# Optimization experiments

Hardware: AMD Instinct MI355X
Metric: run time of the kernel (lower is better)

The kernel has to match this reference:

```python
import jax, jax.numpy as jnp
import numpy as np

NEG_SLOPE = 0.2  # PyG GATConv default negative_slope
BN_EPS = 1e-5


def gat_layer(x, src, dst, W, b, a_src, a_dst, heads, out_ch, concat):
    # x: [N, Fin]; W: [Fin, heads*out_ch]; a_src/a_dst: [heads, out_ch]
    N = x.shape[0]
    h = (x @ W).reshape(N, heads, out_ch)
    s = (h * a_src).sum(-1)            # [N, H]
    d = (h * a_dst).sum(-1)            # [N, H]
    e = jax.nn.leaky_relu(s[src] + d[dst], NEG_SLOPE)   # [E, H]
    # segment softmax over incoming edges of each destination node
    m = jax.ops.segment_max(e, dst, num_segments=N)
    ex = jnp.exp(e - m[dst])
    denom = jax.ops.segment_sum(ex, dst, num_segments=N)
    alpha = ex / (denom[dst] + 1e-16)                   # [E, H]
    out = jax.ops.segment_sum(alpha[:, :, None] * h[src], dst, num_segments=N)  # [N,H,C]
    out = out.reshape(N, heads * out_ch) if concat else out.mean(axis=1)
    return out + b


def batchnorm(x, gamma, beta):
    mu = x.mean(axis=0)
    var = x.var(axis=0)
    return gamma * (x - mu) * jax.lax.rsqrt(var + BN_EPS) + beta


def setup_inputs() -> dict:
    key = jax.random.key(0)
    ks = jax.random.split(key, 24)
    N, E, Fin, Hd, heads, C = 50000, 800000, 128, 64, 4, 2
    wdim = Hd * heads  # 256
    inp = {
        'x': jax.random.normal(ks[0], (N, Fin), jnp.float32),
        'edge_index': jax.random.randint(ks[1], (2, E), 0, N, jnp.int64),
    }
    def glorot(k, shape):
        fan = shape[0] + shape[-1]
        return jax.random.normal(k, shape, jnp.float32) * np.sqrt(2.0 / fan)
    # layer 0: Fin -> heads x Hd (concat)
    inp['W0'] = glorot(ks[2], (Fin, wdim)); inp['b0'] = jnp.zeros((wdim,), jnp.float32)
    inp['asrc0'] = glorot(ks[3], (heads, Hd)); inp['adst0'] = glorot(ks[4], (heads, Hd))
    inp['g0'] = jnp.ones((wdim,), jnp.float32); inp['be0'] = jnp.zeros((wdim,), jnp.float32)
    # layer 1: wdim -> heads x Hd (concat)
    inp['W1'] = glorot(ks[5], (wdim, wdim)); inp['b1'] = jnp.zeros((wdim,), jnp.float32)
    inp['asrc1'] = glorot(ks[6], (heads, Hd)); inp['adst1'] = glorot(ks[7], (heads, Hd))
    inp['g1'] = jnp.ones((wdim,), jnp.float32); inp['be1'] = jnp.zeros((wdim,), jnp.float32)
    # layer 2: wdim -> 1 head x Hd (no concat)
    inp['W2'] = glorot(ks[8], (wdim, Hd)); inp['b2'] = jnp.zeros((Hd,), jnp.float32)
    inp['asrc2'] = glorot(ks[9], (1, Hd)); inp['adst2'] = glorot(ks[10], (1, Hd))
    inp['g2'] = jnp.ones((Hd,), jnp.float32); inp['be2'] = jnp.zeros((Hd,), jnp.float32)
    # classifier: Linear(2*Hd, Hd) -> ReLU -> Linear(Hd, C)
    inp['Wc1'] = glorot(ks[11], (2 * Hd, Hd)); inp['bc1'] = jnp.zeros((Hd,), jnp.float32)
    inp['Wc2'] = glorot(ks[12], (Hd, C)); inp['bc2'] = jnp.zeros((C,), jnp.float32)
    return inp


def reference(x, edge_index, W0, b0, asrc0, adst0, g0, be0,
              W1, b1, asrc1, adst1, g1, be1,
              W2, b2, asrc2, adst2, g2, be2,
              Wc1, bc1, Wc2, bc2):
    N = x.shape[0]
    # add self-loops (PyG GATConv default)
    loops = jnp.arange(N, dtype=edge_index.dtype)
    src = jnp.concatenate([edge_index[0], loops])
    dst = jnp.concatenate([edge_index[1], loops])
    heads, Hd = asrc0.shape[0], asrc0.shape[1]

    h = gat_layer(x, src, dst, W0, b0, asrc0, adst0, heads, Hd, True)
    h = jax.nn.relu(batchnorm(h, g0, be0))
    h = gat_layer(h, src, dst, W1, b1, asrc1, adst1, heads, Hd, True)
    h = jax.nn.relu(batchnorm(h, g1, be1))
    h = gat_layer(h, src, dst, W2, b2, asrc2, adst2, 1, Hd, False)
    h = jax.nn.relu(batchnorm(h, g2, be2))

    pooled = jnp.concatenate([h.mean(axis=0, keepdims=True),
                              h.max(axis=0, keepdims=True)], axis=1)  # [1, 2*Hd]
    z = jax.nn.relu(pooled @ Wc1 + bc1)
    return z @ Wc2 + bc2  # [1, num_classes]
```

## Files before the change

kernel.cpp:

```cpp
#include <hip/hip_runtime.h>


typedef unsigned int uint;
typedef unsigned short ushort;

#define NEG_SLOPE 0.2f
#define BN_EPS 1e-5f
#define NB_RED 256

typedef __attribute__((ext_vector_type(2))) float f32x2;

__device__ __forceinline__ float bf2f(uint u) { return __uint_as_float(u << 16); }
__device__ __forceinline__ ushort f2bf(float f) {
    uint u = __float_as_uint(f);
    u += 0x7fff + ((u >> 16) & 1);
    return (ushort)(u >> 16);
}


__global__ void prep_kernel(const float* __restrict__ x, ushort* __restrict__ xb,
                            int total_real, int total_pad,
                            const float* __restrict__ W0, ushort* __restrict__ w0t,
                            const float* __restrict__ W1, ushort* __restrict__ w1t,
                            const float* __restrict__ W2, ushort* __restrict__ w2t,
                            const int* __restrict__ ei, int* __restrict__ deg, int E) {
    int i = blockIdx.x * blockDim.x + threadIdx.x;
    if (i < total_pad) {
        xb[i] = (i < total_real) ? f2bf(x[i]) : (ushort)0;
        return;
    }
    int j = i - total_pad;
    if (j < 32768) {
        int n = j / 128, k = j - n * 128;
        w0t[j] = f2bf(W0[(size_t)k * 256 + n]);
        return;
    }
    j -= 32768;
    if (j < 65536) {
        int n = j / 256, k = j - n * 256;
        w1t[j] = f2bf(W1[(size_t)k * 256 + n]);
        return;
    }
    j -= 65536;
    if (j < 16384) {
        int n = j / 256, k = j - n * 256;
        w2t[j] = f2bf(W2[(size_t)k * 64 + n]);
        return;
    }
    j -= 16384;
    if (j < E) atomicAdd(&deg[ei[E + j]], 1);
}


__global__ void scan_part(const int* __restrict__ deg, int* __restrict__ offsets,
                          int* __restrict__ bsum, int N) {
    __shared__ int sh[256];
    int t = threadIdx.x;
    int base = blockIdx.x * 1024 + t * 4;
    int v0 = (base + 0 < N) ? deg[base + 0] : 0;
    int v1 = (base + 1 < N) ? deg[base + 1] : 0;
    int v2 = (base + 2 < N) ? deg[base + 2] : 0;
    int v3 = (base + 3 < N) ? deg[base + 3] : 0;
    int s = v0 + v1 + v2 + v3;
    sh[t] = s;
    __syncthreads();
    for (int off = 1; off < 256; off <<= 1) {
        int y = (t >= off) ? sh[t - off] : 0;
        __syncthreads();
        sh[t] += y;
        __syncthreads();
    }
    int p = sh[t] - s;
    if (base + 0 < N) offsets[base + 0] = p;
    p += v0;
    if (base + 1 < N) offsets[base + 1] = p;
    p += v1;
    if (base + 2 < N) offsets[base + 2] = p;
    p += v2;
    if (base + 3 < N) offsets[base + 3] = p;
    if (t == 255) bsum[blockIdx.x] = sh[255];
}

__global__ void scan_top(const int* __restrict__ bsum, int* __restrict__ bexcl,
                         int nb, int* __restrict__ offsets, int N) {
    if (threadIdx.x == 0) {
        int run = 0;
        for (int b = 0; b < nb; ++b) { bexcl[b] = run; run += bsum[b]; }
        offsets[N] = run;
    }
}

__global__ void scan_add(int* __restrict__ offsets, int* __restrict__ cursor,
                         const int* __restrict__ bexcl, int N) {
    int add = bexcl[blockIdx.x];
    int base = blockIdx.x * 1024 + threadIdx.x * 4;
#pragma unroll
    for (int k = 0; k < 4; ++k) {
        int i = base + k;
        if (i < N) { int v = offsets[i] + add; offsets[i] = v; cursor[i] = v; }
    }
}

__global__ void scatter_kernel(const int* __restrict__ ei, int* __restrict__ cursor,
                               int* __restrict__ srcs, int E) {
    int e = blockIdx.x * blockDim.x + threadIdx.x;
    if (e < E) {
        int s = ei[e];
        int d = ei[E + e];
        int p = atomicAdd(&cursor[d], 1);
        srcs[p] = s;
    }
}


typedef __attribute__((ext_vector_type(8))) short bf16x8;
typedef __attribute__((ext_vector_type(4))) float floatx4;

template <int BN, int H>
__launch_bounds__(256)
__global__ void mfma_gemm_bt(const ushort* __restrict__ A, const ushort* __restrict__ Bt,
                             ushort* __restrict__ C, const float* __restrict__ asrc,
                             const float* __restrict__ adst, float* __restrict__ sv,
                             float* __restrict__ dv, int K, int Nn) {
    constexpr int WCOLS = (BN == 128) ? 2 : 1;
    constexpr int WROWS = 4 / WCOLS;
    constexpr int MT = 128 / (WROWS * 16);
    constexpr int NT = BN / (WCOLS * 16);
    constexpr int BCALLS = (BN * 32 * 2) / 4096;

    __shared__ ushort As[128 * 32];
    __shared__ ushort Bs[BN * 32];

    int t = threadIdx.x;
    int w = t >> 6, l = t & 63;

    int rb, cb;
    if (BN == 128) {
        int nbr = (int)gridDim.x >> 1;
        int full = (nbr & ~7) << 1;
        int id = blockIdx.x;
        if (id < full) {
            rb = ((id >> 4) << 3) + (id & 7);
            cb = (id >> 3) & 1;
        } else {
            int o = id - full;
            int rem = nbr & 7;
            rb = (nbr & ~7) + (rem ? (o % rem) : 0);
            cb = rem ? (o / rem) : 0;
        }
    } else {
        rb = blockIdx.x;
        cb = 0;
    }
    int row0 = rb * 128;
    int col0 = cb * BN;
    int wr = (w / WCOLS) * (MT * 16);
    int wc = (w % WCOLS) * (NT * 16);

    floatx4 acc[MT][NT];
#pragma unroll
    for (int mi = 0; mi < MT; ++mi)
#pragma unroll
        for (int ni = 0; ni < NT; ++ni)
#pragma unroll
            for (int r = 0; r < 4; ++r) acc[mi][ni][r] = 0.f;

    int mrow = l & 15;
    int kc = (l >> 4) * 8;

    for (int kt = 0; kt < K; kt += 32) {
#pragma unroll
        for (int c = 0; c < 2; ++c) {
            int idx = c * 256 + t;
            const ushort* gp = A + (size_t)(row0 + (idx >> 2)) * K + kt + (idx & 3) * 8;
            __builtin_amdgcn_global_load_lds(
                (const __attribute__((address_space(1))) void*)gp,
                (__attribute__((address_space(3))) void*)(As + (idx & ~63) * 8),
                16, 0, 0);
        }
#pragma unroll
        for (int c = 0; c < BCALLS; ++c) {
            int idx = c * 256 + t;
            const ushort* gp = Bt + (size_t)(col0 + (idx >> 2)) * K + kt + (idx & 3) * 8;
            __builtin_amdgcn_global_load_lds(
                (const __attribute__((address_space(1))) void*)gp,
                (__attribute__((address_space(3))) void*)(Bs + (idx & ~63) * 8),
                16, 0, 0);
        }
        __syncthreads();

        bf16x8 af[MT], bfr[NT];
#pragma unroll
        for (int mi = 0; mi < MT; ++mi)
            af[mi] = *(const bf16x8*)&As[(wr + mi * 16 + mrow) * 32 + kc];
#pragma unroll
        for (int ni = 0; ni < NT; ++ni)
            bfr[ni] = *(const bf16x8*)&Bs[(wc + ni * 16 + mrow) * 32 + kc];
#pragma unroll
        for (int mi = 0; mi < MT; ++mi)
#pragma unroll
            for (int ni = 0; ni < NT; ++ni)
                acc[mi][ni] = __builtin_amdgcn_mfma_f32_16x16x32_bf16(
                    af[mi], bfr[ni], acc[mi][ni], 0, 0, 0);
        __syncthreads();
    }

#pragma unroll
    for (int mi = 0; mi < MT; ++mi) {
        int rbase = row0 + wr + mi * 16 + (l >> 4) * 4;
#pragma unroll
        for (int ni = 0; ni < NT; ++ni) {
            int col = col0 + wc + ni * 16 + (l & 15);
#pragma unroll
            for (int r = 0; r < 4; ++r)
                C[(size_t)(rbase + r) * Nn + col] = f2bf(acc[mi][ni][r]);
        }
    }

    float av[NT], bv[NT];
#pragma unroll
    for (int ni = 0; ni < NT; ++ni) {
        int ch = col0 + wc + ni * 16 + (l & 15);
        av[ni] = asrc[ch];
        bv[ni] = adst[ch];
    }
    int gh = (col0 + wc) >> 6;
#pragma unroll
    for (int mi = 0; mi < MT; ++mi) {
#pragma unroll
        for (int r = 0; r < 4; ++r) {
            float s = 0.f, d = 0.f;
#pragma unroll
            for (int ni = 0; ni < NT; ++ni) {
                float hv = acc[mi][ni][r];
                s += hv * av[ni];
                d += hv * bv[ni];
            }
#pragma unroll
            for (int m = 8; m >= 1; m >>= 1) {
                s += __shfl_xor(s, m);
                d += __shfl_xor(d, m);
            }
            if ((l & 15) == 0) {
                int row = row0 + wr + mi * 16 + (l >> 4) * 4 + r;
                sv[row * H + gh] = s;
                dv[row * H + gh] = d;
            }
        }
    }
}


#define CAP4 256

#define ACCUMW4(qv_, wt_) { \
    f32x2 wv_ = {(wt_), (wt_)}; \
    uint pr_[4] = {(qv_).x, (qv_).y, (qv_).z, (qv_).w}; \
    _Pragma("unroll") \
    for (int k_ = 0; k_ < 4; ++k_) { \
        f32x2 hv_ = {__uint_as_float(pr_[k_] << 16), \
                     __uint_as_float(pr_[k_] & 0xffff0000u)}; \
        ax[k_] += wv_ * hv_; \
    } }

__launch_bounds__(128)
__global__ void agg4_kernel(const ushort* __restrict__ hb, const float* __restrict__ sv,
                            const float* __restrict__ dv, const int* __restrict__ offsets,
                            const int* __restrict__ srcs, const float* __restrict__ bias,
                            ushort* __restrict__ zb, int N) {
    __shared__ float lsum[4][288];
    __shared__ int   sidx[CAP4];
    __shared__ float swgt[CAP4][4];
    __shared__ float lden[4];

    int i = blockIdx.x;
    int t = threadIdx.x;
    int grp = t >> 5, gl = t & 31;
    int head = gl >> 3;
    int beg = offsets[i], end = offsets[i + 1];
    int cnt = end - beg;
    int scnt = cnt < CAP4 ? cnt : CAP4;

    if (t < 4) lden[t] = 0.f;
    for (int k = t; k < scnt; k += 128) sidx[k] = srcs[beg + k];
    __syncthreads();

    {
        int h = t & 3;
        float dvh = dv[i * 4 + h];
        for (int k4 = t; k4 < scnt * 4; k4 += 128) {
            int k = k4 >> 2;
            float e = sv[sidx[k] * 4 + h] + dvh;
            float wgt = __expf(fminf(fmaxf(e, NEG_SLOPE * e), 60.f));
            swgt[k][h] = wgt;
            atomicAdd(&lden[h], wgt);
        }
    }
    __syncthreads();

    f32x2 ax[4] = {};
    const ushort* hrow = hb + gl * 8;

    int k = grp;
    float wA = 0.f, wB = 0.f;
    uint4 qA = {0, 0, 0, 0}, qB = {0, 0, 0, 0};
    if (k < scnt) {
        int n = sidx[k];
        wA = swgt[k][head];
        qA = *(const uint4*)(hrow + (size_t)n * 256);
    }
    if (k + 4 < scnt) {
        int n = sidx[k + 4];
        wB = swgt[k + 4][head];
        qB = *(const uint4*)(hrow + (size_t)n * 256);
    }
    while (k + 4 < scnt) {
        int kc = k + 8, kd = k + 12;
        float wC = 0.f, wD = 0.f;
        uint4 qC = {0, 0, 0, 0}, qD = {0, 0, 0, 0};
        if (kc < scnt) {
            int n = sidx[kc];
            wC = swgt[kc][head];
            qC = *(const uint4*)(hrow + (size_t)n * 256);
        }
        if (kd < scnt) {
            int n = sidx[kd];
            wD = swgt[kd][head];
            qD = *(const uint4*)(hrow + (size_t)n * 256);
        }
        ACCUMW4(qA, wA);
        ACCUMW4(qB, wB);
        wA = wC; qA = qC;
        wB = wD; qB = qD;
        k += 8;
    }
    if (k < scnt) ACCUMW4(qA, wA);

    if (cnt > CAP4) {
        float d_i = dv[i * 4 + head];
        for (int k2 = CAP4 + grp; k2 < cnt; k2 += 4) {
            int n = srcs[beg + k2];
            float e = sv[n * 4 + head] + d_i;
            float wgt = __expf(fminf(fmaxf(e, NEG_SLOPE * e), 60.f));
            if ((gl & 7) == 0) atomicAdd(&lden[head], wgt);
            uint4 q4 = *(const uint4*)(hrow + (size_t)n * 256);
            ACCUMW4(q4, wgt);
        }
    }

#pragma unroll
    for (int kk = 0; kk < 4; ++kk) {
        lsum[grp][gl * 9 + 2 * kk]     = ax[kk].x;
        lsum[grp][gl * 9 + 2 * kk + 1] = ax[kk].y;
    }
    __syncthreads();

    int h = t >> 5;
    float e_self = sv[i * 4 + h] + dv[i * 4 + h];
    float wself = __expf(fminf(fmaxf(e_self, NEG_SLOPE * e_self), 60.f));
    float dtot = lden[h] + wself + 1e-16f;
    float rden = 1.f / dtot;
    int idx = 2 * t + (t >> 2);
    uint p = *(const uint*)&hb[(size_t)i * 256 + 2 * t];
    float a0 = lsum[0][idx] + lsum[1][idx] + lsum[2][idx] + lsum[3][idx]
             + wself * __uint_as_float(p << 16);
    float a1 = lsum[0][idx + 1] + lsum[1][idx + 1] + lsum[2][idx + 1]
             + lsum[3][idx + 1] + wself * __uint_as_float(p & 0xffff0000u);
    a0 = a0 * rden + bias[2 * t];
    a1 = a1 * rden + bias[2 * t + 1];
    *(uint*)&zb[(size_t)i * 256 + 2 * t] = (uint)f2bf(a0) | ((uint)f2bf(a1) << 16);
}


#define CAP1 256

#define ACCUMW1(qv_, wt_) { \
    f32x2 wv_ = {(wt_), (wt_)}; \
    f32x2 h0_ = {__uint_as_float((qv_).x << 16), __uint_as_float((qv_).x & 0xffff0000u)}; \
    f32x2 h1_ = {__uint_as_float((qv_).y << 16), __uint_as_float((qv_).y & 0xffff0000u)}; \
    ax[0] += wv_ * h0_; \
    ax[1] += wv_ * h1_; }

__launch_bounds__(64)
__global__ void agg1_kernel(const ushort* __restrict__ hb, const float* __restrict__ sv,
                            const float* __restrict__ dv, const int* __restrict__ offsets,
                            const int* __restrict__ srcs, const float* __restrict__ bias,
                            ushort* __restrict__ zb, int N) {
    __shared__ int   sidx[CAP1];
    __shared__ float swgt[CAP1];

    int i = blockIdx.x;
    int l = threadIdx.x;
    int grp = l >> 4, gl = l & 15;
    int beg = offsets[i], end = offsets[i + 1];
    int cnt = end - beg;
    int scnt = cnt < CAP1 ? cnt : CAP1;

    float d_i = dv[i];

    for (int k = l; k < scnt; k += 64) sidx[k] = srcs[beg + k];
    __syncthreads();

    float denp = 0.f;
    for (int k = l; k < scnt; k += 64) {
        float e = sv[sidx[k]] + d_i;
        float wgt = __expf(fminf(fmaxf(e, NEG_SLOPE * e), 60.f));
        swgt[k] = wgt;
        denp += wgt;
    }
    __syncthreads();
    float den = denp;
#pragma unroll
    for (int m = 32; m >= 1; m >>= 1) den += __shfl_xor(den, m);

    f32x2 ax[2] = {};
    const ushort* hrow = hb + gl * 4;

    int k = grp;
    float wA = 0.f, wB = 0.f;
    uint2 qA = {0, 0}, qB = {0, 0};
    if (k < scnt) {
        int n = sidx[k];
        wA = swgt[k];
        qA = *(const uint2*)(hrow + (size_t)n * 64);
    }
    if (k + 4 < scnt) {
        int n = sidx[k + 4];
        wB = swgt[k + 4];
        qB = *(const uint2*)(hrow + (size_t)n * 64);
    }
    while (k + 4 < scnt) {
        int kc = k + 8, kd = k + 12;
        float wC = 0.f, wD = 0.f;
        uint2 qC = {0, 0}, qD = {0, 0};
        if (kc < scnt) {
            int n = sidx[kc];
            wC = swgt[kc];
            qC = *(const uint2*)(hrow + (size_t)n * 64);
        }
        if (kd < scnt) {
            int n = sidx[kd];
            wD = swgt[kd];
            qD = *(const uint2*)(hrow + (size_t)n * 64);
        }
        ACCUMW1(qA, wA);
        ACCUMW1(qB, wB);
        wA = wC; qA = qC;
        wB = wD; qB = qD;
        k += 8;
    }
    if (k < scnt) ACCUMW1(qA, wA);

    if (cnt > CAP1) {
        float dslow = 0.f;
        for (int k2 = CAP1 + grp; k2 < cnt; k2 += 4) {
            int n = srcs[beg + k2];
            float e = sv[n] + d_i;
            float wgt = __expf(fminf(fmaxf(e, NEG_SLOPE * e), 60.f));
            if (gl == 0) dslow += wgt;
            uint2 q2 = *(const uint2*)(hrow + (size_t)n * 64);
            ACCUMW1(q2, wgt);
        }
#pragma unroll
        for (int m = 32; m >= 1; m >>= 1) dslow += __shfl_xor(dslow, m);
        den += dslow;
    }

    float a4[4] = {ax[0].x, ax[0].y, ax[1].x, ax[1].y};
#pragma unroll
    for (int kk = 0; kk < 4; ++kk) {
        a4[kk] += __shfl_xor(a4[kk], 16);
        a4[kk] += __shfl_xor(a4[kk], 32);
    }

    if (l < 16) {
        float e_self = sv[i] + d_i;
        float wself = __expf(fminf(fmaxf(e_self, NEG_SLOPE * e_self), 60.f));
        float rden = 1.f / (den + wself + 1e-16f);
        uint2 q = *(const uint2*)&hb[(size_t)i * 64 + gl * 4];
        float a0 = (a4[0] + wself * bf2f(q.x & 0xffffu)) * rden + bias[gl * 4 + 0];
        float a1 = (a4[1] + wself * bf2f(q.x >> 16)) * rden + bias[gl * 4 + 1];
        float a2 = (a4[2] + wself * bf2f(q.y & 0xffffu)) * rden + bias[gl * 4 + 2];
        float a3 = (a4[3] + wself * bf2f(q.y >> 16)) * rden + bias[gl * 4 + 3];
        uint2 o;
        o.x = (uint)f2bf(a0) | ((uint)f2bf(a1) << 16);
        o.y = (uint)f2bf(a2) | ((uint)f2bf(a3) << 16);
        *(uint2*)&zb[(size_t)i * 64 + gl * 4] = o;
    }
}


template <int F>
__launch_bounds__(256)
__global__ void bn_stats_kernel(const ushort* __restrict__ x, float* __restrict__ ps,
                                float* __restrict__ pq, int N) {
    constexpr int OCT = F / 8;
    __shared__ float lds_s[F], lds_q[F];
    int t = threadIdx.x;
    if (t < F) { lds_s[t] = 0.f; lds_q[t] = 0.f; }
    __syncthreads();

    float s[8] = {}, q[8] = {};
    int total8 = N * F / 8;
    for (int idx = blockIdx.x * 256 + t; idx < total8; idx += NB_RED * 256) {
        uint4 v = ((const uint4*)x)[idx];
        uint pr[4] = {v.x, v.y, v.z, v.w};
#pragma unroll
        for (int k = 0; k < 4; ++k) {
            float a = bf2f(pr[k] & 0xffffu);
            float b = bf2f(pr[k] >> 16);
            s[2 * k] += a;     q[2 * k] += a * a;
            s[2 * k + 1] += b; q[2 * k + 1] += b * b;
        }
    }
    int co = t % OCT;
#pragma unroll
    for (int j = 0; j < 8; ++j) {
        atomicAdd(&lds_s[co * 8 + j], s[j]);
        atomicAdd(&lds_q[co * 8 + j], q[j]);
    }
    __syncthreads();
    if (t < F) {
        ps[blockIdx.x * F + t] = lds_s[t];
        pq[blockIdx.x * F + t] = lds_q[t];
    }
}

__global__ void bn_final_kernel(const float* __restrict__ ps, const float* __restrict__ pq,
                                const float* __restrict__ g, const float* __restrict__ be,
                                float* __restrict__ scale, float* __restrict__ shift,
                                int N, int F) {
    int t = threadIdx.x;
    if (t < F) {
        float s = 0.f, q = 0.f;
        for (int b = 0; b < NB_RED; ++b) { s += ps[b * F + t]; q += pq[b * F + t]; }
        float mean = s / (float)N;
        float var = q / (float)N - mean * mean;
        float sc = g[t] * rsqrtf(var + BN_EPS);
        scale[t] = sc;
        shift[t] = be[t] - sc * mean;
    }
}

__global__ void bn_apply_kernel(uint* __restrict__ x, const float* __restrict__ scale,
                                const float* __restrict__ shift, int totalPairs, int Fmask) {
    int i = blockIdx.x * blockDim.x + threadIdx.x;
    if (i < totalPairs) {
        uint p = x[i];
        int c0 = (2 * i) & Fmask;
        float v0 = fmaxf(bf2f(p & 0xffffu) * scale[c0] + shift[c0], 0.f);
        float v1 = fmaxf(bf2f(p >> 16) * scale[c0 + 1] + shift[c0 + 1], 0.f);
        x[i] = (uint)f2bf(v0) | ((uint)f2bf(v1) << 16);
    }
}


__launch_bounds__(256)
__global__ void pool_kernel(const ushort* __restrict__ y, const float* __restrict__ scale,
                            const float* __restrict__ shift, float* __restrict__ psum,
                            float* __restrict__ pmax, int N) {
    constexpr int F = 64, OCT = 8;
    __shared__ float lds_s[F];
    __shared__ uint lds_m[F];
    int t = threadIdx.x;
    if (t < F) { lds_s[t] = 0.f; lds_m[t] = 0u; }
    __syncthreads();

    int co = t % OCT;
    float sc[8], sh[8];
#pragma unroll
    for (int j = 0; j < 8; ++j) { sc[j] = scale[co * 8 + j]; sh[j] = shift[co * 8 + j]; }

    float s[8] = {}, m[8] = {};
    int total8 = N * F / 8;
    for (int idx = blockIdx.x * 256 + t; idx < total8; idx += NB_RED * 256) {
        uint4 v = ((const uint4*)y)[idx];
        uint pr[4] = {v.x, v.y, v.z, v.w};
#pragma unroll
        for (int k = 0; k < 4; ++k) {
            float a = fmaxf(bf2f(pr[k] & 0xffffu) * sc[2 * k] + sh[2 * k], 0.f);
            float b = fmaxf(bf2f(pr[k] >> 16) * sc[2 * k + 1] + sh[2 * k + 1], 0.f);
            s[2 * k] += a;     m[2 * k] = fmaxf(m[2 * k], a);
            s[2 * k + 1] += b; m[2 * k + 1] = fmaxf(m[2 * k + 1], b);
        }
    }
#pragma unroll
    for (int j = 0; j < 8; ++j) {
        atomicAdd(&lds_s[co * 8 + j], s[j]);
        atomicMax(&lds_m[co * 8 + j], __float_as_uint(m[j]));
    }
    __syncthreads();
    if (t < F) {
        psum[blockIdx.x * F + t] = lds_s[t];
        pmax[blockIdx.x * F + t] = __uint_as_float(lds_m[t]);
    }
}

__global__ void classify_kernel(const float* __restrict__ psum, const float* __restrict__ pmax,
                                const float* __restrict__ Wc1, const float* __restrict__ bc1,
                                const float* __restrict__ Wc2, const float* __restrict__ bc2,
                                float* __restrict__ out, int N) {
    __shared__ float pooled[128];
    __shared__ float z[64];
    int t = threadIdx.x;
    if (t < 64) {
        float s = 0.f;
        for (int b = 0; b < NB_RED; ++b) s += psum[b * 64 + t];
        pooled[t] = s / (float)N;
    } else {
        int c = t - 64;
        float m = 0.f;
        for (int b = 0; b < NB_RED; ++b) m = fmaxf(m, pmax[b * 64 + c]);
        pooled[t] = m;
    }
    __syncthreads();
    if (t < 64) {
        float a = bc1[t];
        for (int k = 0; k < 128; ++k) a += pooled[k] * Wc1[k * 64 + t];
        z[t] = a > 0.f ? a : 0.f;
    }
    __syncthreads();
    if (t < 2) {
        float a = bc2[t];
        for (int j = 0; j < 64; ++j) a += z[j] * Wc2[j * 2 + t];
        out[t] = a;
    }
}


extern "C" void kernel_launch(void* const* d_in, const int* in_sizes, int n_in,
                              void* d_out, int out_size, void* d_ws, size_t ws_size,
                              hipStream_t stream) {
    const float* x   = (const float*)d_in[0];
    const int*   ei  = (const int*)d_in[1];
    const float* W0  = (const float*)d_in[2];  const float* b0  = (const float*)d_in[3];
    const float* as0 = (const float*)d_in[4];  const float* ad0 = (const float*)d_in[5];
    const float* g0  = (const float*)d_in[6];  const float* be0 = (const float*)d_in[7];
    const float* W1  = (const float*)d_in[8];  const float* b1  = (const float*)d_in[9];
    const float* as1 = (const float*)d_in[10]; const float* ad1 = (const float*)d_in[11];
    const float* g1  = (const float*)d_in[12]; const float* be1 = (const float*)d_in[13];
    const float* W2  = (const float*)d_in[14]; const float* b2  = (const float*)d_in[15];
    const float* as2 = (const float*)d_in[16]; const float* ad2 = (const float*)d_in[17];
    const float* g2  = (const float*)d_in[18]; const float* be2 = (const float*)d_in[19];
    const float* Wc1 = (const float*)d_in[20]; const float* bc1 = (const float*)d_in[21];
    const float* Wc2 = (const float*)d_in[22]; const float* bc2 = (const float*)d_in[23];
    float* out = (float*)d_out;

    const int N = in_sizes[0] / 128;
    const int E = in_sizes[1] / 2;
    const int Mpad = ((N + 127) / 128) * 128;
    const int NB_SCAN = (N + 1023) / 1024;
    const int NBROW = Mpad / 128;

    char* ws = (char*)d_ws;
    size_t o = 0;
    auto alloc = [&](size_t bytes) -> void* {
        void* p = ws + o;
        o = (o + bytes + 255) & ~(size_t)255;
        return p;
    };
    int*    deg     = (int*)alloc((size_t)N * 4);
    int*    offsets = (int*)alloc((size_t)(N + 1) * 4);
    int*    cursor  = (int*)alloc((size_t)N * 4);
    int*    srcs    = (int*)alloc((size_t)E * 4);
    int*    bsum    = (int*)alloc((size_t)NB_SCAN * 4);
    int*    bexcl   = (int*)alloc((size_t)NB_SCAN * 4);
    ushort* xb      = (ushort*)alloc((size_t)Mpad * 128 * 2);
    ushort* w0t     = (ushort*)alloc((size_t)256 * 128 * 2);
    ushort* w1t     = (ushort*)alloc((size_t)256 * 256 * 2);
    ushort* w2t     = (ushort*)alloc((size_t)64 * 256 * 2);
    ushort* hb      = (ushort*)alloc((size_t)Mpad * 256 * 2);
    ushort* zb      = (ushort*)alloc((size_t)Mpad * 256 * 2);
    float*  sv      = (float*)alloc((size_t)Mpad * 4 * 4);
    float*  dv      = (float*)alloc((size_t)Mpad * 4 * 4);
    float*  ps      = (float*)alloc((size_t)NB_RED * 256 * 4);
    float*  pq      = (float*)alloc((size_t)NB_RED * 256 * 4);
    float*  scale   = (float*)alloc(256 * 4);
    float*  shift   = (float*)alloc(256 * 4);
    float*  psum    = (float*)alloc((size_t)NB_RED * 64 * 4);
    float*  pmax    = (float*)alloc((size_t)NB_RED * 64 * 4);

    (void)hipMemsetAsync(deg, 0, (size_t)N * 4, stream);
    int prep_total = Mpad * 128 + 32768 + 65536 + 16384 + E;
    prep_kernel<<<(prep_total + 255) / 256, 256, 0, stream>>>(
        x, xb, N * 128, Mpad * 128, W0, w0t, W1, w1t, W2, w2t, ei, deg, E);

    scan_part<<<NB_SCAN, 256, 0, stream>>>(deg, offsets, bsum, N);
    scan_top<<<1, 64, 0, stream>>>(bsum, bexcl, NB_SCAN, offsets, N);
    scan_add<<<NB_SCAN, 256, 0, stream>>>(offsets, cursor, bexcl, N);
    scatter_kernel<<<(E + 255) / 256, 256, 0, stream>>>(ei, cursor, srcs, E);

    {
        mfma_gemm_bt<128, 4><<<NBROW * 2, 256, 0, stream>>>(xb, w0t, hb, as0, ad0, sv, dv, 128, 256);
        agg4_kernel<<<N, 128, 0, stream>>>(hb, sv, dv, offsets, srcs, b0, zb, N);
        bn_stats_kernel<256><<<NB_RED, 256, 0, stream>>>(zb, ps, pq, N);
        bn_final_kernel<<<1, 256, 0, stream>>>(ps, pq, g0, be0, scale, shift, N, 256);
        bn_apply_kernel<<<(N * 128 + 255) / 256, 256, 0, stream>>>((uint*)zb, scale, shift,
                                                                   N * 128, 255);
    }
    {
        mfma_gemm_bt<128, 4><<<NBROW * 2, 256, 0, stream>>>(zb, w1t, hb, as1, ad1, sv, dv, 256, 256);
        agg4_kernel<<<N, 128, 0, stream>>>(hb, sv, dv, offsets, srcs, b1, zb, N);
        bn_stats_kernel<256><<<NB_RED, 256, 0, stream>>>(zb, ps, pq, N);
        bn_final_kernel<<<1, 256, 0, stream>>>(ps, pq, g1, be1, scale, shift, N, 256);
        bn_apply_kernel<<<(N * 128 + 255) / 256, 256, 0, stream>>>((uint*)zb, scale, shift,
                                                                   N * 128, 255);
    }
    {
        mfma_gemm_bt<64, 1><<<NBROW, 256, 0, stream>>>(zb, w2t, hb, as2, ad2, sv, dv, 256, 64);
        agg1_kernel<<<N, 64, 0, stream>>>(hb, sv, dv, offsets, srcs, b2, zb, N);
        bn_stats_kernel<64><<<NB_RED, 256, 0, stream>>>(zb, ps, pq, N);
        bn_final_kernel<<<1, 64, 0, stream>>>(ps, pq, g2, be2, scale, shift, N, 64);
    }

    pool_kernel<<<NB_RED, 256, 0, stream>>>(zb, scale, shift, psum, pmax, N);
    classify_kernel<<<1, 128, 0, stream>>>(psum, pmax, Wc1, bc1, Wc2, bc2, out, N);
}
```

Measured before the change: 588.0 us.

## Aggregate four destination nodes per block with one sub-group per node

The attention-aggregation kernels now give each 32-lane (or 16-lane) sub-group its own destination node, so each block handles four nodes instead of one. This removes the cross-group shared-memory reduction and its extra barrier, cuts the launch count by a factor of four, and switches to a four-deep software-prefetched gather loop. The shared neighbour cache shrinks from 256 to 64 entries, so high-degree nodes fall back to a serial slow path. The average degree is about 17, which makes imbalance between the four sub-groups of a block the main risk.

Result: no change. 588.1 us (+0.0%).

```diff
diff --git a/kernel.cpp b/kernel.cpp
--- a/kernel.cpp
+++ b/kernel.cpp
@@ -251,7 +251,7 @@
 }
 
 
-#define CAP4 256
+#define CAP4 64
 
 #define ACCUMW4(qv_, wt_) { \
     f32x2 wv_ = {(wt_), (wt_)}; \
@@ -263,116 +263,99 @@
         ax[k_] += wv_ * hv_; \
     } }
 
+#define LDQ4(kk_, wv_, qv_) { \
+    int kq_ = (kk_); \
+    if (kq_ < scnt) { \
+        int nq_ = sidx[sub][kq_]; \
+        wv_ = swgt[sub][kq_][head]; \
+        qv_ = *(const uint4*)(hrow + (size_t)nq_ * 256); \
+    } else { wv_ = 0.f; qv_.x = 0; qv_.y = 0; qv_.z = 0; qv_.w = 0; } }
+
 __launch_bounds__(128)
 __global__ void agg4_kernel(const ushort* __restrict__ hb, const float* __restrict__ sv,
                             const float* __restrict__ dv, const int* __restrict__ offsets,
                             const int* __restrict__ srcs, const float* __restrict__ bias,
                             ushort* __restrict__ zb, int N) {
-    __shared__ float lsum[4][288];
-    __shared__ int   sidx[CAP4];
-    __shared__ float swgt[CAP4][4];
-    __shared__ float lden[4];
-
-    int i = blockIdx.x;
-    int t = threadIdx.x;
-    int grp = t >> 5, gl = t & 31;
+    __shared__ int   sidx[4][CAP4];
+    __shared__ float swgt[4][CAP4][4];
+    __shared__ float lden[4][4];
+
+    int t = threadIdx.x;
+    int sub = t >> 5, gl = t & 31;
     int head = gl >> 3;
-    int beg = offsets[i], end = offsets[i + 1];
-    int cnt = end - beg;
+    int i = blockIdx.x * 4 + sub;
+    bool valid = i < N;
+
+    int beg = 0, cnt = 0;
+    if (valid) { beg = offsets[i]; cnt = offsets[i + 1] - beg; }
     int scnt = cnt < CAP4 ? cnt : CAP4;
 
-    if (t < 4) lden[t] = 0.f;
-    for (int k = t; k < scnt; k += 128) sidx[k] = srcs[beg + k];
+    if (gl < 4) lden[sub][gl] = 0.f;
+    for (int k = gl; k < scnt; k += 32) sidx[sub][k] = srcs[beg + k];
     __syncthreads();
 
     {
-        int h = t & 3;
-        float dvh = dv[i * 4 + h];
-        for (int k4 = t; k4 < scnt * 4; k4 += 128) {
-            int k = k4 >> 2;
-            float e = sv[sidx[k] * 4 + h] + dvh;
+        int h = gl & 3;
+        float dvh = valid ? dv[i * 4 + h] : 0.f;
+        float denp = 0.f;
+        for (int idx = gl; idx < scnt * 4; idx += 32) {
+            int k = idx >> 2;
+            float e = sv[sidx[sub][k] * 4 + h] + dvh;
             float wgt = __expf(fminf(fmaxf(e, NEG_SLOPE * e), 60.f));
-            swgt[k][h] = wgt;
-            atomicAdd(&lden[h], wgt);
-        }
+            swgt[sub][k][h] = wgt;
+            denp += wgt;
+        }
+        atomicAdd(&lden[sub][h], denp);
     }
     __syncthreads();
 
     f32x2 ax[4] = {};
     const ushort* hrow = hb + gl * 8;
 
-    int k = grp;
-    float wA = 0.f, wB = 0.f;
-    uint4 qA = {0, 0, 0, 0}, qB = {0, 0, 0, 0};
-    if (k < scnt) {
-        int n = sidx[k];
-        wA = swgt[k][head];
-        qA = *(const uint4*)(hrow + (size_t)n * 256);
-    }
-    if (k + 4 < scnt) {
-        int n = sidx[k + 4];
-        wB = swgt[k + 4][head];
-        qB = *(const uint4*)(hrow + (size_t)n * 256);
-    }
-    while (k + 4 < scnt) {
-        int kc = k + 8, kd = k + 12;
-        float wC = 0.f, wD = 0.f;
-        uint4 qC = {0, 0, 0, 0}, qD = {0, 0, 0, 0};
-        if (kc < scnt) {
-            int n = sidx[kc];
-            wC = swgt[kc][head];
-            qC = *(const uint4*)(hrow + (size_t)n * 256);
-        }
-        if (kd < scnt) {
-            int n = sidx[kd];
-            wD = swgt[kd][head];
-            qD = *(const uint4*)(hrow + (size_t)n * 256);
-        }
-        ACCUMW4(qA, wA);
-        ACCUMW4(qB, wB);
-        wA = wC; qA = qC;
-        wB = wD; qB = qD;
-        k += 8;
-    }
-    if (k < scnt) ACCUMW4(qA, wA);
+    float w0, w1, w2, w3;
+    uint4 q0, q1, q2, q3;
+    LDQ4(0, w0, q0); LDQ4(1, w1, q1); LDQ4(2, w2, q2); LDQ4(3, w3, q3);
+    for (int k = 0; k < scnt; k += 4) {
+        float v0 = w0, v1 = w1, v2 = w2, v3 = w3;
+        uint4 p0 = q0, p1 = q1, p2 = q2, p3 = q3;
+        LDQ4(k + 4, w0, q0); LDQ4(k + 5, w1, q1);
+        LDQ4(k + 6, w2, q2); LDQ4(k + 7, w3, q3);
+        ACCUMW4(p0, v0);
+        ACCUMW4(p1, v1);
+        ACCUMW4(p2, v2);
+        ACCUMW4(p3, v3);
+    }
 
     if (cnt > CAP4) {
         float d_i = dv[i * 4 + head];
-        for (int k2 = CAP4 + grp; k2 < cnt; k2 += 4) {
+        for (int k2 = CAP4; k2 < cnt; ++k2) {
             int n = srcs[beg + k2];
             float e = sv[n * 4 + head] + d_i;
             float wgt = __expf(fminf(fmaxf(e, NEG_SLOPE * e), 60.f));
-            if ((gl & 7) == 0) atomicAdd(&lden[head], wgt);
+            if ((gl & 7) == 0) atomicAdd(&lden[sub][head], wgt);
             uint4 q4 = *(const uint4*)(hrow + (size_t)n * 256);
             ACCUMW4(q4, wgt);
         }
     }
 
-#pragma unroll
-    for (int kk = 0; kk < 4; ++kk) {
-        lsum[grp][gl * 9 + 2 * kk]     = ax[kk].x;
-        lsum[grp][gl * 9 + 2 * kk + 1] = ax[kk].y;
-    }
-    __syncthreads();
-
-    int h = t >> 5;
-    float e_self = sv[i * 4 + h] + dv[i * 4 + h];
-    float wself = __expf(fminf(fmaxf(e_self, NEG_SLOPE * e_self), 60.f));
-    float dtot = lden[h] + wself + 1e-16f;
-    float rden = 1.f / dtot;
-    int idx = 2 * t + (t >> 2);
-    uint p = *(const uint*)&hb[(size_t)i * 256 + 2 * t];
-    float a0 = lsum[0][idx] + lsum[1][idx] + lsum[2][idx] + lsum[3][idx]
-             + wself * __uint_as_float(p << 16);
-    float a1 = lsum[0][idx + 1] + lsum[1][idx + 1] + lsum[2][idx + 1]
-             + lsum[3][idx + 1] + wself * __uint_as_float(p & 0xffff0000u);
-    a0 = a0 * rden + bias[2 * t];
-    a1 = a1 * rden + bias[2 * t + 1];
-    *(uint*)&zb[(size_t)i * 256 + 2 * t] = (uint)f2bf(a0) | ((uint)f2bf(a1) << 16);
-}
-
-
-#define CAP1 256
+    if (valid) {
+        float e_self = sv[i * 4 + head] + dv[i * 4 + head];
+        float wself = __expf(fminf(fmaxf(e_self, NEG_SLOPE * e_self), 60.f));
+        uint4 qs = *(const uint4*)&hb[(size_t)i * 256 + gl * 8];
+        ACCUMW4(qs, wself);
+        float rden = 1.f / (lden[sub][head] + wself + 1e-16f);
+        const float* bb = bias + gl * 8;
+        uint4 o;
+        o.x = (uint)f2bf(ax[0].x * rden + bb[0]) | ((uint)f2bf(ax[0].y * rden + bb[1]) << 16);
+        o.y = (uint)f2bf(ax[1].x * rden + bb[2]) | ((uint)f2bf(ax[1].y * rden + bb[3]) << 16);
+        o.z = (uint)f2bf(ax[2].x * rden + bb[4]) | ((uint)f2bf(ax[2].y * rden + bb[5]) << 16);
+        o.w = (uint)f2bf(ax[3].x * rden + bb[6]) | ((uint)f2bf(ax[3].y * rden + bb[7]) << 16);
+        *(uint4*)&zb[(size_t)i * 256 + gl * 8] = o;
+    }
+}
+
+
+#define CAP1 64
 
 #define ACCUMW1(qv_, wt_) { \
     f32x2 wv_ = {(wt_), (wt_)}; \
@@ -381,110 +364,87 @@
     ax[0] += wv_ * h0_; \
     ax[1] += wv_ * h1_; }
 
+#define LDQ1(kk_, wv_, qv_) { \
+    int kq_ = (kk_); \
+    if (kq_ < scnt) { \
+        int nq_ = sidx[sub][kq_]; \
+        wv_ = swgt[sub][kq_]; \
+        qv_ = *(const uint2*)(hrow + (size_t)nq_ * 64); \
+    } else { wv_ = 0.f; qv_.x = 0; qv_.y = 0; } }
+
 __launch_bounds__(64)
 __global__ void agg1_kernel(const ushort* __restrict__ hb, const float* __restrict__ sv,
                             const float* __restrict__ dv, const int* __restrict__ offsets,
                             const int* __restrict__ srcs, const float* __restrict__ bias,
                             ushort* __restrict__ zb, int N) {
-    __shared__ int   sidx[CAP1];
-    __shared__ float swgt[CAP1];
-
-    int i = blockIdx.x;
-    int l = threadIdx.x;
-    int grp = l >> 4, gl = l & 15;
-    int beg = offsets[i], end = offsets[i + 1];
-    int cnt = end - beg;
+    __shared__ int   sidx[4][CAP1];
+    __shared__ float swgt[4][CAP1];
+    __shared__ float lden[4];
+
+    int t = threadIdx.x;
+    int sub = t >> 4, gl = t & 15;
+    int i = blockIdx.x * 4 + sub;
+    bool valid = i < N;
+
+    int beg = 0, cnt = 0;
+    if (valid) { beg = offsets[i]; cnt = offsets[i + 1] - beg; }
     int scnt = cnt < CAP1 ? cnt : CAP1;
 
-    float d_i = dv[i];
-
-    for (int k = l; k < scnt; k += 64) sidx[k] = srcs[beg + k];
-    __syncthreads();
-
-    float denp = 0.f;
-    for (int k = l; k < scnt; k += 64) {
-        float e = sv[sidx[k]] + d_i;
-        float wgt = __expf(fminf(fmaxf(e, NEG_SLOPE * e), 60.f));
-        swgt[k] = wgt;
-        denp += wgt;
-    }
-    __syncthreads();
-    float den = denp;
-#pragma unroll
-    for (int m = 32; m >= 1; m >>= 1) den += __shfl_xor(den, m);
+    if (gl == 0) lden[sub] = 0.f;
+    for (int k = gl; k < scnt; k += 16) sidx[sub][k] = srcs[beg + k];
+    __syncthreads();
+
+    float d_i = valid ? dv[i] : 0.f;
+    {
+        float denp = 0.f;
+        for (int k = gl; k < scnt; k += 16) {
+            float e = sv[sidx[sub][k]] + d_i;
+            float wgt = __expf(fminf(fmaxf(e, NEG_SLOPE * e), 60.f));
+            swgt[sub][k] = wgt;
+            denp += wgt;
+        }
+        atomicAdd(&lden[sub], denp);
+    }
+    __syncthreads();
 
     f32x2 ax[2] = {};
     const ushort* hrow = hb + gl * 4;
 
-    int k = grp;
-    float wA = 0.f, wB = 0.f;
-    uint2 qA = {0, 0}, qB = {0, 0};
-    if (k < scnt) {
-        int n = sidx[k];
-        wA = swgt[k];
-        qA = *(const uint2*)(hrow + (size_t)n * 64);
-    }
-    if (k + 4 < scnt) {
-        int n = sidx[k + 4];
-        wB = swgt[k + 4];
-        qB = *(const uint2*)(hrow + (size_t)n * 64);
-    }
-    while (k + 4 < scnt) {
-        int kc = k + 8, kd = k + 12;
-        float wC = 0.f, wD = 0.f;
-        uint2 qC = {0, 0}, qD = {0, 0};
-        if (kc < scnt) {
-            int n = sidx[kc];
-            wC = swgt[kc];
-            qC = *(const uint2*)(hrow + (size_t)n * 64);
-        }
-        if (kd < scnt) {
-            int n = sidx[kd];
-            wD = swgt[kd];
-            qD = *(const uint2*)(hrow + (size_t)n * 64);
-        }
-        ACCUMW1(qA, wA);
-        ACCUMW1(qB, wB);
-        wA = wC; qA = qC;
-        wB = wD; qB = qD;
-        k += 8;
-    }
-    if (k < scnt) ACCUMW1(qA, wA);
+    float w0, w1, w2, w3;
+    uint2 q0, q1, q2, q3;
+    LDQ1(0, w0, q0); LDQ1(1, w1, q1); LDQ1(2, w2, q2); LDQ1(3, w3, q3);
+    for (int k = 0; k < scnt; k += 4) {
+        float v0 = w0, v1 = w1, v2 = w2, v3 = w3;
+        uint2 p0 = q0, p1 = q1, p2 = q2, p3 = q3;
+        LDQ1(k + 4, w0, q0); LDQ1(k + 5, w1, q1);
+        LDQ1(k + 6, w2, q2); LDQ1(k + 7, w3, q3);
+        ACCUMW1(p0, v0);
+        ACCUMW1(p1, v1);
+        ACCUMW1(p2, v2);
+        ACCUMW1(p3, v3);
+    }
 
     if (cnt > CAP1) {
-        float dslow = 0.f;
-        for (int k2 = CAP1 + grp; k2 < cnt; k2 += 4) {
+        for (int k2 = CAP1; k2 < cnt; ++k2) {
             int n = srcs[beg + k2];
             float e = sv[n] + d_i;
             float wgt = __expf(fminf(fmaxf(e, NEG_SLOPE * e), 60.f));
-            if (gl == 0) dslow += wgt;
-            uint2 q2 = *(const uint2*)(hrow + (size_t)n * 64);
-            ACCUMW1(q2, wgt);
-        }
-#pragma unroll
-        for (int m = 32; m >= 1; m >>= 1) dslow += __shfl_xor(dslow, m);
-        den += dslow;
-    }
-
-    float a4[4] = {ax[0].x, ax[0].y, ax[1].x, ax[1].y};
-#pragma unroll
-    for (int kk = 0; kk < 4; ++kk) {
-        a4[kk] += __shfl_xor(a4[kk], 16);
-        a4[kk] += __shfl_xor(a4[kk], 32);
-    }
-
-    if (l < 16) {
+            if (gl == 0) atomicAdd(&lden[sub], wgt);
+            uint2 q2v = *(const uint2*)(hrow + (size_t)n * 64);
+            ACCUMW1(q2v, wgt);
+        }
+    }
+
+    if (valid) {
         float e_self = sv[i] + d_i;
         float wself = __expf(fminf(fmaxf(e_self, NEG_SLOPE * e_self), 60.f));
-        float rden = 1.f / (den + wself + 1e-16f);
-        uint2 q = *(const uint2*)&hb[(size_t)i * 64 + gl * 4];
-        float a0 = (a4[0] + wself * bf2f(q.x & 0xffffu)) * rden + bias[gl * 4 + 0];
-        float a1 = (a4[1] + wself * bf2f(q.x >> 16)) * rden + bias[gl * 4 + 1];
-        float a2 = (a4[2] + wself * bf2f(q.y & 0xffffu)) * rden + bias[gl * 4 + 2];
-        float a3 = (a4[3] + wself * bf2f(q.y >> 16)) * rden + bias[gl * 4 + 3];
+        uint2 qs = *(const uint2*)&hb[(size_t)i * 64 + gl * 4];
+        ACCUMW1(qs, wself);
+        float rden = 1.f / (lden[sub] + wself + 1e-16f);
+        const float* bb = bias + gl * 4;
         uint2 o;
-        o.x = (uint)f2bf(a0) | ((uint)f2bf(a1) << 16);
-        o.y = (uint)f2bf(a2) | ((uint)f2bf(a3) << 16);
+        o.x = (uint)f2bf(ax[0].x * rden + bb[0]) | ((uint)f2bf(ax[0].y * rden + bb[1]) << 16);
+        o.y = (uint)f2bf(ax[1].x * rden + bb[2]) | ((uint)f2bf(ax[1].y * rden + bb[3]) << 16);
         *(uint2*)&zb[(size_t)i * 64 + gl * 4] = o;
     }
 }
@@ -651,6 +611,7 @@
     const int Mpad = ((N + 127) / 128) * 128;
     const int NB_SCAN = (N + 1023) / 1024;
     const int NBROW = Mpad / 128;
+    const int NB_AGG = (N + 3) / 4;
 
     char* ws = (char*)d_ws;
     size_t o = 0;
@@ -692,7 +653,7 @@
 
     {
         mfma_gemm_bt<128, 4><<<NBROW * 2, 256, 0, stream>>>(xb, w0t, hb, as0, ad0, sv, dv, 128, 256);
-        agg4_kernel<<<N, 128, 0, stream>>>(hb, sv, dv, offsets, srcs, b0, zb, N);
+        agg4_kernel<<<NB_AGG, 128, 0, stream>>>(hb, sv, dv, offsets, srcs, b0, zb, N);
         bn_stats_kernel<256><<<NB_RED, 256, 0, stream>>>(zb, ps, pq, N);
         bn_final_kernel<<<1, 256, 0, stream>>>(ps, pq, g0, be0, scale, shift, N, 256);
         bn_apply_kernel<<<(N * 128 + 255) / 256, 256, 0, stream>>>((uint*)zb, scale, shift,
@@ -700,7 +661,7 @@
     }
     {
         mfma_gemm_bt<128, 4><<<NBROW * 2, 256, 0, stream>>>(zb, w1t, hb, as1, ad1, sv, dv, 256, 256);
-        agg4_kernel<<<N, 128, 0, stream>>>(hb, sv, dv, offsets, srcs, b1, zb, N);
+        agg4_kernel<<<NB_AGG, 128, 0, stream>>>(hb, sv, dv, offsets, srcs, b1, zb, N);
         bn_stats_kernel<256><<<NB_RED, 256, 0, stream>>>(zb, ps, pq, N);
         bn_final_kernel<<<1, 256, 0, stream>>>(ps, pq, g1, be1, scale, shift, N, 256);
         bn_apply_kernel<<<(N * 128 + 255) / 256, 256, 0, stream>>>((uint*)zb, scale, shift,
@@ -708,7 +669,7 @@
     }
     {
         mfma_gemm_bt<64, 1><<<NBROW, 256, 0, stream>>>(zb, w2t, hb, as2, ad2, sv, dv, 256, 64);
-        agg1_kernel<<<N, 64, 0, stream>>>(hb, sv, dv, offsets, srcs, b2, zb, N);
+        agg1_kernel<<<NB_AGG, 64, 0, stream>>>(hb, sv, dv, offsets, srcs, b2, zb, N);
         bn_stats_kernel<64><<<NB_RED, 256, 0, stream>>>(zb, ps, pq, N);
         bn_final_kernel<<<1, 64, 0, stream>>>(ps, pq, g2, be2, scale, shift, N, 64);
     }
```
